# Optimization experiments

Hardware: AMD Instinct MI355X
Metric: run time of the kernel (lower is better)

The kernel has to match this reference:

```python
import jax, jax.numpy as jnp
import numpy as np

B, T, D = 4, 4096, 1024
N, L = 2048, 768
H = 16
EPS = 1e-5

def layernorm(x, g, b):
    mu = jnp.mean(x, axis=-1, keepdims=True)
    var = jnp.mean((x - mu) ** 2, axis=-1, keepdims=True)
    return (x - mu) * jax.lax.rsqrt(var + EPS) * g + b

def setup_inputs() -> dict:
    key = jax.random.key(0)
    ks = jax.random.split(key, 8)
    s_d = 1.0 / np.sqrt(D)
    s_l = 1.0 / np.sqrt(L)
    return {
        "x1": jax.random.normal(ks[0], (B, T, D), jnp.float32),
        "x2": jax.random.normal(ks[1], (B, N, L), jnp.float32),
        "Wq": jax.random.normal(ks[2], (D, D), jnp.float32) * s_d,
        "bq": jnp.zeros((D,), jnp.float32),
        "Wk": jax.random.normal(ks[3], (L, D), jnp.float32) * s_l,
        "bk": jnp.zeros((D,), jnp.float32),
        "Wv": jax.random.normal(ks[4], (L, D), jnp.float32) * s_l,
        "bv": jnp.zeros((D,), jnp.float32),
        "Wh": jax.random.normal(ks[5], (D, D), jnp.float32) * s_d,
        "bh": jnp.zeros((D,), jnp.float32),
        "g1": jnp.ones((D,), jnp.float32),
        "b1": jnp.zeros((D,), jnp.float32),
        "g2": jnp.ones((L,), jnp.float32),
        "b2": jnp.zeros((L,), jnp.float32),
    }

def reference(x1, x2, Wq, bq, Wk, bk, Wv, bv, Wh, bh, g1, b1, g2, b2):
    nx1 = layernorm(x1, g1, b1)
    nx2 = layernorm(x2, g2, b2)
    q = (nx1 @ Wq + bq).reshape(B, T, H, D // H)
    k = (nx2 @ Wk + bk).reshape(B, N, H, D // H)
    v = (nx2 @ Wv + bv).reshape(B, N, H, D // H)
    q = jax.nn.softmax(q, axis=-1)
    k = jax.nn.softmax(k, axis=-1)
    # dropout p=0 -> identity
    attn = jnp.einsum('bnhd,bnhl->bhdl', k, v)          # [B,H,dh,dh]
    y = jnp.einsum('bthd,bhdl->bthl', q, attn).reshape(B, T, D)
    return x1 @ Wh + bh + y
```

## Files before the change

### kernel.cpp

```cpp
#include <hip/hip_runtime.h>


#define DEV __device__ __forceinline__

typedef unsigned short bf16_t;
typedef __attribute__((ext_vector_type(8))) __bf16 bf16x8;
typedef __attribute__((ext_vector_type(8))) unsigned short ushort8;
typedef __attribute__((ext_vector_type(4))) float f32x4;

DEV unsigned short f2bf(float f) {
  unsigned int u = __float_as_uint(f);
  unsigned int r = 0x7FFFu + ((u >> 16) & 1u);
  return (unsigned short)((u + r) >> 16);
}
DEV float bf2f(unsigned short u) { return __uint_as_float(((unsigned int)u) << 16); }

DEV void gld16(const void* g, void* l) {
  __builtin_amdgcn_global_load_lds((__attribute__((address_space(1))) void*)g,
                                   (__attribute__((address_space(3))) void*)l, 16, 0, 0);
}

__global__ __launch_bounds__(256) void prep_kernel(
    const float* __restrict__ Wq, const float* __restrict__ Wk,
    const float* __restrict__ Wv, const float* __restrict__ Wh,
    bf16_t* __restrict__ Wqf, bf16_t* __restrict__ Wkf,
    bf16_t* __restrict__ Wvf, bf16_t* __restrict__ Whf,
    const float* __restrict__ x1, const float* __restrict__ g1,
    const float* __restrict__ b1, bf16_t* __restrict__ nx1f,
    bf16_t* __restrict__ x1f,
    const float* __restrict__ x2, const float* __restrict__ g2,
    const float* __restrict__ b2, bf16_t* __restrict__ nx2f) {
  __shared__ __align__(16) char smem[16 * 1032 * 2];
  __shared__ float murs[16][2];
  int blk = blockIdx.x, tid = threadIdx.x;

  if (blk < 3584) {
    int t = blk;
    const float* src; bf16_t* dst; int KB;
    if (t < 1024)      { src = Wq; dst = Wqf; KB = 32; }
    else if (t < 1792) { src = Wk; dst = Wkf; KB = 24; t -= 1024; }
    else if (t < 2560) { src = Wv; dst = Wvf; KB = 24; t -= 1792; }
    else               { src = Wh; dst = Whf; KB = 32; t -= 2560; }
    int tk = t >> 5, tn = t & 31;
    float (*tile)[33] = (float(*)[33])smem;
    int tx = tid & 31, ty = tid >> 5;
#pragma unroll
    for (int i = 0; i < 4; ++i) {
      int r = ty + i * 8;
      tile[r][tx] = src[(size_t)(tk * 32 + r) * 1024 + tn * 32 + tx];
    }
    __syncthreads();
    if (tid < 128) {
      int rt = tid >> 6, p = (tid >> 4) & 3, ri = tid & 15;
      ushort8 v;
#pragma unroll
      for (int ko = 0; ko < 8; ++ko)
        v[ko] = f2bf(tile[p * 8 + ko][rt * 16 + ri]);
      size_t off = ((size_t)(tn * 2 + rt) * KB + tk) * 512 + p * 128 + ri * 8;
      *(ushort8*)&dst[off] = v;
    }
    return;
  }

  if (blk < 4608) {
    bf16_t* stash = (bf16_t*)smem;
    int rt = blk - 3584;
    {
      int rowl = tid >> 4, ci = tid & 15;
      size_t base = ((size_t)rt * 16 + rowl) * 1024;
      float s = 0.f, s2 = 0.f;
#pragma unroll
      for (int j = 0; j < 16; ++j) {
        int k0 = ci * 4 + j * 64;
        float4 f = *(const float4*)&x1[base + k0];
        s += f.x + f.y + f.z + f.w;
        s2 += f.x * f.x + f.y * f.y + f.z * f.z + f.w * f.w;
        ushort4 u;
        u.x = f2bf(f.x); u.y = f2bf(f.y); u.z = f2bf(f.z); u.w = f2bf(f.w);
        *(ushort4*)&stash[rowl * 1032 + k0] = u;
      }
#pragma unroll
      for (int off = 1; off < 16; off <<= 1) {
        s  += __shfl_xor(s, off);
        s2 += __shfl_xor(s2, off);
      }
      if (ci == 0) {
        float mu = s * (1.0f / 1024.0f);
        float var = s2 * (1.0f / 1024.0f) - mu * mu;
        murs[rowl][0] = mu;
        murs[rowl][1] = rsqrtf(var + 1e-5f);
      }
    }
    __syncthreads();
    {
      int ri = tid & 15, pg = tid >> 4;
      float mu = murs[ri][0], rs = murs[ri][1];
#pragma unroll
      for (int t = 0; t < 8; ++t) {
        int P = pg * 8 + t;
        ushort8 raw = *(const ushort8*)&stash[ri * 1032 + P * 8];
        float4 ga = *(const float4*)&g1[P * 8], gb = *(const float4*)&g1[P * 8 + 4];
        float4 ba = *(const float4*)&b1[P * 8], bb = *(const float4*)&b1[P * 8 + 4];
        float gv[8] = {ga.x, ga.y, ga.z, ga.w, gb.x, gb.y, gb.z, gb.w};
        float bv[8] = {ba.x, ba.y, ba.z, ba.w, bb.x, bb.y, bb.z, bb.w};
        ushort8 nv;
#pragma unroll
        for (int ko = 0; ko < 8; ++ko)
          nv[ko] = f2bf((bf2f(raw[ko]) - mu) * rs * gv[ko] + bv[ko]);
        size_t off = ((size_t)rt * 32 + (P >> 2)) * 512 + (P & 3) * 128 + ri * 8;
        *(ushort8*)&nx1f[off] = nv;
        *(ushort8*)&x1f[off] = raw;
      }
    }
    return;
  }

  {
    bf16_t* stash = (bf16_t*)smem;
    int rt = blk - 4608;
    {
      int rowl = tid >> 4, ci = tid & 15;
      size_t base = ((size_t)rt * 16 + rowl) * 768;
      float s = 0.f, s2 = 0.f;
#pragma unroll
      for (int j = 0; j < 12; ++j) {
        int k0 = ci * 4 + j * 64;
        float4 f = *(const float4*)&x2[base + k0];
        s += f.x + f.y + f.z + f.w;
        s2 += f.x * f.x + f.y * f.y + f.z * f.z + f.w * f.w;
        ushort4 u;
        u.x = f2bf(f.x); u.y = f2bf(f.y); u.z = f2bf(f.z); u.w = f2bf(f.w);
        *(ushort4*)&stash[rowl * 776 + k0] = u;
      }
#pragma unroll
      for (int off = 1; off < 16; off <<= 1) {
        s  += __shfl_xor(s, off);
        s2 += __shfl_xor(s2, off);
      }
      if (ci == 0) {
        float mu = s * (1.0f / 768.0f);
        float var = s2 * (1.0f / 768.0f) - mu * mu;
        murs[rowl][0] = mu;
        murs[rowl][1] = rsqrtf(var + 1e-5f);
      }
    }
    __syncthreads();
    {
      int ri = tid & 15, pg = tid >> 4;
      float mu = murs[ri][0], rs = murs[ri][1];
#pragma unroll
      for (int t = 0; t < 6; ++t) {
        int P = pg * 6 + t;
        ushort8 raw = *(const ushort8*)&stash[ri * 776 + P * 8];
        float4 ga = *(const float4*)&g2[P * 8], gb = *(const float4*)&g2[P * 8 + 4];
        float4 ba = *(const float4*)&b2[P * 8], bb = *(const float4*)&b2[P * 8 + 4];
        float gv[8] = {ga.x, ga.y, ga.z, ga.w, gb.x, gb.y, gb.z, gb.w};
        float bv[8] = {ba.x, ba.y, ba.z, ba.w, bb.x, bb.y, bb.z, bb.w};
        ushort8 nv;
#pragma unroll
        for (int ko = 0; ko < 8; ++ko)
          nv[ko] = f2bf((bf2f(raw[ko]) - mu) * rs * gv[ko] + bv[ko]);
        size_t off = ((size_t)rt * 24 + (P >> 2)) * 512 + (P & 3) * 128 + ri * 8;
        *(ushort8*)&nx2f[off] = nv;
      }
    }
  }
}

__global__ __launch_bounds__(256, 2) void gemm_qkv_kernel(
    const bf16_t* __restrict__ nx1f, const bf16_t* __restrict__ Wqf,
    const float* __restrict__ bq, bf16_t* __restrict__ qout,
    const bf16_t* __restrict__ nx2f, const bf16_t* __restrict__ Wkf,
    const float* __restrict__ bk, bf16_t* __restrict__ kout,
    const bf16_t* __restrict__ Wvf, const float* __restrict__ bv,
    bf16_t* __restrict__ vout) {
  __shared__ bf16_t Bs[2 * 16 * 512];
  int id = blockIdx.x;
  const bf16_t *A, *BT; const float* bias; bf16_t* out;
  int nk, bm, bn, do_softmax;
  if (id < 512) {
    A = nx1f; BT = Wqf; bias = bq; out = qout; nk = 32;
    bm = id & 127; bn = id >> 7; do_softmax = 1;
  } else if (id < 768) {
    id -= 512; A = nx2f; BT = Wkf; bias = bk; out = kout; nk = 24;
    bm = id & 63; bn = id >> 6; do_softmax = 1;
  } else {
    id -= 768; A = nx2f; BT = Wvf; bias = bv; out = vout; nk = 24;
    bm = id & 63; bn = id >> 6; do_softmax = 0;
  }
  int tid = threadIdx.x, lane = tid & 63, wid = tid >> 6;
  int wm = wid & 1, wn = wid >> 1;

  const bf16_t* ap[4];
#pragma unroll
  for (int mi = 0; mi < 4; ++mi)
    ap[mi] = A + ((size_t)(bm * 8 + wm * 4 + mi) * nk) * 512 + lane * 8;
  const bf16_t* sp[4];
#pragma unroll
  for (int i = 0; i < 4; ++i)
    sp[i] = BT + ((size_t)(bn * 16 + wid * 4 + i) * nk) * 512 + lane * 8;

  f32x4 acc[4][8];
#pragma unroll
  for (int i = 0; i < 4; ++i)
#pragma unroll
    for (int j = 0; j < 8; ++j) acc[i][j] = {0.f, 0.f, 0.f, 0.f};

  bf16x8 acur[4], anxt[4];
#pragma unroll
  for (int i = 0; i < 4; ++i)
    gld16(sp[i], (void*)&Bs[(wid * 4 + i) * 512 + lane * 8]);
#pragma unroll
  for (int mi = 0; mi < 4; ++mi) acur[mi] = *(const bf16x8*)ap[mi];

  for (int kt = 0; kt < nk; ++kt) {
    int cb = kt & 1;
    if (kt + 1 < nk) {
      int nb = cb ^ 1;
#pragma unroll
      for (int i = 0; i < 4; ++i)
        gld16(sp[i] + (kt + 1) * 512, (void*)&Bs[nb * 8192 + (wid * 4 + i) * 512 + lane * 8]);
#pragma unroll
      for (int mi = 0; mi < 4; ++mi) anxt[mi] = *(const bf16x8*)(ap[mi] + (kt + 1) * 512);
      asm volatile("s_waitcnt vmcnt(8)\n\ts_barrier" ::: "memory");
    } else {
      asm volatile("s_waitcnt vmcnt(0)\n\ts_barrier" ::: "memory");
    }
    bf16x8 bfr[8];
#pragma unroll
    for (int ni = 0; ni < 8; ++ni)
      bfr[ni] = *(const bf16x8*)&Bs[cb * 8192 + (wn * 8 + ni) * 512 + lane * 8];
#pragma unroll
    for (int mi = 0; mi < 4; ++mi)
#pragma unroll
      for (int ni = 0; ni < 8; ++ni)
        acc[mi][ni] = __builtin_amdgcn_mfma_f32_16x16x32_bf16(acur[mi], bfr[ni], acc[mi][ni], 0, 0, 0);
    asm volatile("s_waitcnt lgkmcnt(0)\n\ts_barrier" ::: "memory");
#pragma unroll
    for (int mi = 0; mi < 4; ++mi) acur[mi] = anxt[mi];
  }

  int colg0 = bn * 256 + wn * 128;
  float bvv[8];
#pragma unroll
  for (int ni = 0; ni < 8; ++ni) bvv[ni] = bias[colg0 + ni * 16 + (lane & 15)];
#pragma unroll
  for (int mi = 0; mi < 4; ++mi) {
#pragma unroll
    for (int r = 0; r < 4; ++r) {
      int row = bm * 128 + wm * 64 + mi * 16 + (lane >> 4) * 4 + r;
      float vx[8];
#pragma unroll
      for (int ni = 0; ni < 8; ++ni) vx[ni] = acc[mi][ni][r] + bvv[ni];
      if (do_softmax) {
#pragma unroll
        for (int g = 0; g < 2; ++g) {
          float ssum = 0.f;
#pragma unroll
          for (int j = 0; j < 4; ++j) { vx[g * 4 + j] = __expf(vx[g * 4 + j]); ssum += vx[g * 4 + j]; }
#pragma unroll
          for (int off = 1; off < 16; off <<= 1) ssum += __shfl_xor(ssum, off);
          float inv = 1.0f / ssum;
#pragma unroll
          for (int j = 0; j < 4; ++j) vx[g * 4 + j] *= inv;
        }
      }
#pragma unroll
      for (int ni = 0; ni < 8; ++ni)
        out[(size_t)row * 1024 + colg0 + ni * 16 + (lane & 15)] = f2bf(vx[ni]);
    }
  }
}

__global__ __launch_bounds__(256) void attn_partial_kernel(
    const bf16_t* __restrict__ kq, const bf16_t* __restrict__ vq,
    float* __restrict__ part) {
  int bh = blockIdx.x >> 3, c = blockIdx.x & 7;
  int b = bh >> 4, h = bh & 15;
  int tid = threadIdx.x, lane = tid & 63, wid = tid >> 6;
  __shared__ bf16_t Kt[64][40];
  __shared__ bf16_t Vt[64][40];
  f32x4 acc[4];
#pragma unroll
  for (int ni = 0; ni < 4; ++ni) acc[ni] = {0.f, 0.f, 0.f, 0.f};
  int nl = tid & 31, d0 = (tid >> 5) * 8;
  int m = lane & 15, kp = lane >> 4;

  for (int s = 0; s < 8; ++s) {
    int n = c * 256 + s * 32 + nl;
    size_t goff = ((size_t)(b * 2048 + n)) * 1024 + h * 64 + d0;
    ushort8 lk = *(const ushort8*)&kq[goff];
    ushort8 lv = *(const ushort8*)&vq[goff];
    __syncthreads();
#pragma unroll
    for (int j = 0; j < 8; ++j) {
      Kt[d0 + j][nl] = lk[j];
      Vt[d0 + j][nl] = lv[j];
    }
    __syncthreads();
    bf16x8 af = *(const bf16x8*)&Kt[wid * 16 + m][kp * 8];
#pragma unroll
    for (int ni = 0; ni < 4; ++ni) {
      bf16x8 bf = *(const bf16x8*)&Vt[ni * 16 + m][kp * 8];
      acc[ni] = __builtin_amdgcn_mfma_f32_16x16x32_bf16(af, bf, acc[ni], 0, 0, 0);
    }
  }
#pragma unroll
  for (int ni = 0; ni < 4; ++ni)
#pragma unroll
    for (int r = 0; r < 4; ++r) {
      int d = wid * 16 + kp * 4 + r;
      int l = ni * 16 + m;
      part[(((size_t)bh * 8 + c) * 64 + d) * 64 + l] = acc[ni][r];
    }
}

__global__ __launch_bounds__(256) void attn_finalize_kernel(
    const float* __restrict__ part, bf16_t* __restrict__ attnT) {
  int bh = blockIdx.x, tid = threadIdx.x;
  for (int t = tid; t < 4096; t += 256) {
    int d = t >> 6, l = t & 63;
    float s = 0.f;
#pragma unroll
    for (int c = 0; c < 8; ++c)
      s += part[(((size_t)bh * 8 + c) * 64 + d) * 64 + l];
    attnT[((size_t)bh * 64 + l) * 64 + d] = f2bf(s);
  }
}

__global__ __launch_bounds__(256, 2) void gemm_final_kernel(
    const bf16_t* __restrict__ x1f, const bf16_t* __restrict__ Whf,
    const float* __restrict__ bias, const bf16_t* __restrict__ qb,
    const bf16_t* __restrict__ attnT, float* __restrict__ out) {
  __shared__ bf16_t Bs[2 * 16 * 512];
  const int nk = 32;
  int tid = threadIdx.x;
  int bm = blockIdx.x, bn = blockIdx.y;
  int lane = tid & 63, wid = tid >> 6;
  int wm = wid & 1, wn = wid >> 1;
  int b = bm >> 5;
  int klane = (lane >> 4) * 8;

  const bf16_t* ap[4];
#pragma unroll
  for (int mi = 0; mi < 4; ++mi)
    ap[mi] = x1f + ((size_t)(bm * 8 + wm * 4 + mi) * nk) * 512 + lane * 8;
  const bf16_t* sp[4];
#pragma unroll
  for (int i = 0; i < 4; ++i)
    sp[i] = Whf + ((size_t)(bn * 16 + wid * 4 + i) * nk) * 512 + lane * 8;

  f32x4 acc[4][8];
#pragma unroll
  for (int i = 0; i < 4; ++i)
#pragma unroll
    for (int j = 0; j < 8; ++j) acc[i][j] = {0.f, 0.f, 0.f, 0.f};

  bf16x8 acur[4], anxt[4];
#pragma unroll
  for (int i = 0; i < 4; ++i)
    gld16(sp[i], (void*)&Bs[(wid * 4 + i) * 512 + lane * 8]);
#pragma unroll
  for (int mi = 0; mi < 4; ++mi) acur[mi] = *(const bf16x8*)ap[mi];

  for (int kt = 0; kt < nk; ++kt) {
    int cb = kt & 1;
    if (kt + 1 < nk) {
      int nb = cb ^ 1;
#pragma unroll
      for (int i = 0; i < 4; ++i)
        gld16(sp[i] + (kt + 1) * 512, (void*)&Bs[nb * 8192 + (wid * 4 + i) * 512 + lane * 8]);
#pragma unroll
      for (int mi = 0; mi < 4; ++mi) anxt[mi] = *(const bf16x8*)(ap[mi] + (kt + 1) * 512);
      asm volatile("s_waitcnt vmcnt(8)\n\ts_barrier" ::: "memory");
    } else {
      asm volatile("s_waitcnt vmcnt(0)\n\ts_barrier" ::: "memory");
    }
    bf16x8 bfr[8];
#pragma unroll
    for (int ni = 0; ni < 8; ++ni)
      bfr[ni] = *(const bf16x8*)&Bs[cb * 8192 + (wn * 8 + ni) * 512 + lane * 8];
#pragma unroll
    for (int mi = 0; mi < 4; ++mi)
#pragma unroll
      for (int ni = 0; ni < 8; ++ni)
        acc[mi][ni] = __builtin_amdgcn_mfma_f32_16x16x32_bf16(acur[mi], bfr[ni], acc[mi][ni], 0, 0, 0);
    asm volatile("s_waitcnt lgkmcnt(0)\n\ts_barrier" ::: "memory");
#pragma unroll
    for (int mi = 0; mi < 4; ++mi) acur[mi] = anxt[mi];
  }

  {
    int h0 = bn * 4 + wn * 2;
#pragma unroll
    for (int k2 = 0; k2 < 2; ++k2) {
      bf16x8 aq[2][4], bt[8];
#pragma unroll
      for (int g = 0; g < 2; ++g)
#pragma unroll
        for (int mi = 0; mi < 4; ++mi)
          aq[g][mi] = *(const bf16x8*)(qb
              + (size_t)(bm * 128 + wm * 64 + mi * 16 + (lane & 15)) * 1024
              + (h0 + g) * 64 + k2 * 32 + klane);
#pragma unroll
      for (int ni = 0; ni < 8; ++ni)
        bt[ni] = *(const bf16x8*)(attnT
            + ((size_t)(b * 16 + h0 + (ni >> 2)) * 64 + (ni & 3) * 16 + (lane & 15)) * 64
            + k2 * 32 + klane);
#pragma unroll
      for (int mi = 0; mi < 4; ++mi)
#pragma unroll
        for (int ni = 0; ni < 8; ++ni)
          acc[mi][ni] = __builtin_amdgcn_mfma_f32_16x16x32_bf16(aq[ni >> 2][mi], bt[ni], acc[mi][ni], 0, 0, 0);
    }
  }

  int colg0 = bn * 256 + wn * 128;
  float bvv[8];
#pragma unroll
  for (int ni = 0; ni < 8; ++ni) bvv[ni] = bias[colg0 + ni * 16 + (lane & 15)];
#pragma unroll
  for (int mi = 0; mi < 4; ++mi)
#pragma unroll
    for (int r = 0; r < 4; ++r) {
      int row = bm * 128 + wm * 64 + mi * 16 + (lane >> 4) * 4 + r;
#pragma unroll
      for (int ni = 0; ni < 8; ++ni)
        out[(size_t)row * 1024 + colg0 + ni * 16 + (lane & 15)] = acc[mi][ni][r] + bvv[ni];
    }
}

extern "C" void kernel_launch(void* const* d_in, const int* in_sizes, int n_in,
                              void* d_out, int out_size, void* d_ws, size_t ws_size,
                              hipStream_t stream) {
  const float* x1 = (const float*)d_in[0];
  const float* x2 = (const float*)d_in[1];
  const float* Wq = (const float*)d_in[2];
  const float* bq = (const float*)d_in[3];
  const float* Wk = (const float*)d_in[4];
  const float* bk = (const float*)d_in[5];
  const float* Wv = (const float*)d_in[6];
  const float* bv = (const float*)d_in[7];
  const float* Wh = (const float*)d_in[8];
  const float* bh = (const float*)d_in[9];
  const float* g1 = (const float*)d_in[10];
  const float* b1 = (const float*)d_in[11];
  const float* g2 = (const float*)d_in[12];
  const float* b2 = (const float*)d_in[13];
  float* out = (float*)d_out;

  char* w = (char*)d_ws;
  bf16_t* nx1f = (bf16_t*)w; w += (size_t)16384 * 1024 * 2;
  bf16_t* x1f  = (bf16_t*)w; w += (size_t)16384 * 1024 * 2;
  bf16_t* nx2f = (bf16_t*)w; w += (size_t)8192 * 768 * 2;
  bf16_t* Wqf  = (bf16_t*)w; w += (size_t)1024 * 1024 * 2;
  bf16_t* Wkf  = (bf16_t*)w; w += (size_t)1024 * 768 * 2;
  bf16_t* Wvf  = (bf16_t*)w; w += (size_t)1024 * 768 * 2;
  bf16_t* Whf  = (bf16_t*)w; w += (size_t)1024 * 1024 * 2;
  bf16_t* qb   = (bf16_t*)w; w += (size_t)16384 * 1024 * 2;
  bf16_t* kbuf = (bf16_t*)w; w += (size_t)8192 * 1024 * 2;
  bf16_t* vbuf = (bf16_t*)w; w += (size_t)8192 * 1024 * 2;
  float*  part = (float*)w;  w += (size_t)64 * 8 * 64 * 64 * 4;
  bf16_t* attnT = (bf16_t*)w; w += (size_t)64 * 64 * 64 * 2;

  prep_kernel<<<dim3(5120), dim3(256), 0, stream>>>(
      Wq, Wk, Wv, Wh, Wqf, Wkf, Wvf, Whf,
      x1, g1, b1, nx1f, x1f, x2, g2, b2, nx2f);
  gemm_qkv_kernel<<<dim3(1024), dim3(256), 0, stream>>>(
      nx1f, Wqf, bq, qb, nx2f, Wkf, bk, kbuf, Wvf, bv, vbuf);
  attn_partial_kernel<<<dim3(512), dim3(256), 0, stream>>>(kbuf, vbuf, part);
  attn_finalize_kernel<<<dim3(64), dim3(256), 0, stream>>>(part, attnT);
  gemm_final_kernel<<<dim3(128, 4), dim3(256), 0, stream>>>(x1f, Whf, bh, qb, attnT, out);
}
```

Before: 299.3 us.

## Fuse attention partial and finalize kernels into one per-head kernel

Replaces the two-pass K^T V computation (512 blocks writing fp32 partials, then a 64-block reduction) with a single kernel of 64 blocks of 512 threads. Each block covers one (batch, head) and splits the sequence across two thread groups. Each group prefetches the next K/V tile into registers before the MFMA step. The two groups' accumulators are combined in shared memory, and the result is written directly as transposed bf16. This removes one launch and the fp32 partial buffer round trip, but cuts the grid to 64 blocks that each run 32 serial iterations, which lowers parallelism on a GPU with many CUs.

Result: slower. 322.9 us (+7.9%).

```diff
diff --git a/kernel.cpp b/kernel.cpp
--- a/kernel.cpp
+++ b/kernel.cpp
@@ -272,59 +272,75 @@
   }
 }
 
-__global__ __launch_bounds__(256) void attn_partial_kernel(
+__global__ __launch_bounds__(512) void attn_kernel(
     const bf16_t* __restrict__ kq, const bf16_t* __restrict__ vq,
-    float* __restrict__ part) {
-  int bh = blockIdx.x >> 3, c = blockIdx.x & 7;
+    bf16_t* __restrict__ attnT) {
+  __shared__ __align__(16) char smem[20480];
+  int bh = blockIdx.x;
   int b = bh >> 4, h = bh & 15;
-  int tid = threadIdx.x, lane = tid & 63, wid = tid >> 6;
-  __shared__ bf16_t Kt[64][40];
-  __shared__ bf16_t Vt[64][40];
+  int tid = threadIdx.x;
+  int g = tid >> 8, tl = tid & 255;
+  int lane = tid & 63, wid = (tid >> 6) & 3;
+  bf16_t* KT = (bf16_t*)(smem + g * 10240);
+  bf16_t* VT = KT + 2560;
+  float* Pt = (float*)smem;
+
+  int nr = tl >> 3, col = (tl & 7) * 8;
+  int m = lane & 15, kp = lane >> 4;
+
   f32x4 acc[4];
 #pragma unroll
   for (int ni = 0; ni < 4; ++ni) acc[ni] = {0.f, 0.f, 0.f, 0.f};
-  int nl = tid & 31, d0 = (tid >> 5) * 8;
-  int m = lane & 15, kp = lane >> 4;
-
-  for (int s = 0; s < 8; ++s) {
-    int n = c * 256 + s * 32 + nl;
-    size_t goff = ((size_t)(b * 2048 + n)) * 1024 + h * 64 + d0;
-    ushort8 lk = *(const ushort8*)&kq[goff];
-    ushort8 lv = *(const ushort8*)&vq[goff];
+
+  size_t gbase = ((size_t)(b * 2048 + g * 1024 + nr)) * 1024 + h * 64 + col;
+  ushort8 ck = *(const ushort8*)&kq[gbase];
+  ushort8 cv = *(const ushort8*)&vq[gbase];
+
+  for (int s = 0; s < 32; ++s) {
+    if (s) __syncthreads();
+#pragma unroll
+    for (int j = 0; j < 8; ++j) {
+      KT[(col + j) * 40 + nr] = (bf16_t)ck[j];
+      VT[(col + j) * 40 + nr] = (bf16_t)cv[j];
+    }
+    if (s + 1 < 32) {
+      size_t go = gbase + (size_t)(s + 1) * 32 * 1024;
+      ck = *(const ushort8*)&kq[go];
+      cv = *(const ushort8*)&vq[go];
+    }
     __syncthreads();
-#pragma unroll
-    for (int j = 0; j < 8; ++j) {
-      Kt[d0 + j][nl] = lk[j];
-      Vt[d0 + j][nl] = lv[j];
-    }
-    __syncthreads();
-    bf16x8 af = *(const bf16x8*)&Kt[wid * 16 + m][kp * 8];
+    bf16x8 af = *(const bf16x8*)&KT[(wid * 16 + m) * 40 + kp * 8];
 #pragma unroll
     for (int ni = 0; ni < 4; ++ni) {
-      bf16x8 bf = *(const bf16x8*)&Vt[ni * 16 + m][kp * 8];
+      bf16x8 bf = *(const bf16x8*)&VT[(ni * 16 + m) * 40 + kp * 8];
       acc[ni] = __builtin_amdgcn_mfma_f32_16x16x32_bf16(af, bf, acc[ni], 0, 0, 0);
     }
   }
-#pragma unroll
-  for (int ni = 0; ni < 4; ++ni)
-#pragma unroll
-    for (int r = 0; r < 4; ++r) {
-      int d = wid * 16 + kp * 4 + r;
-      int l = ni * 16 + m;
-      part[(((size_t)bh * 8 + c) * 64 + d) * 64 + l] = acc[ni][r];
-    }
-}
-
-__global__ __launch_bounds__(256) void attn_finalize_kernel(
-    const float* __restrict__ part, bf16_t* __restrict__ attnT) {
-  int bh = blockIdx.x, tid = threadIdx.x;
-  for (int t = tid; t < 4096; t += 256) {
-    int d = t >> 6, l = t & 63;
-    float s = 0.f;
-#pragma unroll
-    for (int c = 0; c < 8; ++c)
-      s += part[(((size_t)bh * 8 + c) * 64 + d) * 64 + l];
-    attnT[((size_t)bh * 64 + l) * 64 + d] = f2bf(s);
+  __syncthreads();
+  if (g == 0) {
+#pragma unroll
+    for (int ni = 0; ni < 4; ++ni)
+#pragma unroll
+      for (int r = 0; r < 4; ++r)
+        Pt[(ni * 16 + m) * 68 + wid * 16 + kp * 4 + r] = acc[ni][r];
+  }
+  __syncthreads();
+  if (g == 1) {
+#pragma unroll
+    for (int ni = 0; ni < 4; ++ni)
+#pragma unroll
+      for (int r = 0; r < 4; ++r)
+        Pt[(ni * 16 + m) * 68 + wid * 16 + kp * 4 + r] += acc[ni][r];
+  }
+  __syncthreads();
+  {
+    int l = tid >> 3, d0 = (tid & 7) * 8;
+    float4 pa = *(const float4*)&Pt[l * 68 + d0];
+    float4 pb = *(const float4*)&Pt[l * 68 + d0 + 4];
+    ushort8 o;
+    o[0] = f2bf(pa.x); o[1] = f2bf(pa.y); o[2] = f2bf(pa.z); o[3] = f2bf(pa.w);
+    o[4] = f2bf(pb.x); o[5] = f2bf(pb.y); o[6] = f2bf(pb.z); o[7] = f2bf(pb.w);
+    *(ushort8*)&attnT[((size_t)bh * 64 + l) * 64 + d0] = o;
   }
 }
 
@@ -460,7 +476,6 @@
   bf16_t* qb   = (bf16_t*)w; w += (size_t)16384 * 1024 * 2;
   bf16_t* kbuf = (bf16_t*)w; w += (size_t)8192 * 1024 * 2;
   bf16_t* vbuf = (bf16_t*)w; w += (size_t)8192 * 1024 * 2;
-  float*  part = (float*)w;  w += (size_t)64 * 8 * 64 * 64 * 4;
   bf16_t* attnT = (bf16_t*)w; w += (size_t)64 * 64 * 64 * 2;
 
   prep_kernel<<<dim3(5120), dim3(256), 0, stream>>>(
@@ -468,7 +483,6 @@
       x1, g1, b1, nx1f, x1f, x2, g2, b2, nx2f);
   gemm_qkv_kernel<<<dim3(1024), dim3(256), 0, stream>>>(
       nx1f, Wqf, bq, qb, nx2f, Wkf, bk, kbuf, Wvf, bv, vbuf);
-  attn_partial_kernel<<<dim3(512), dim3(256), 0, stream>>>(kbuf, vbuf, part);
-  attn_finalize_kernel<<<dim3(64), dim3(256), 0, stream>>>(part, attnT);
+  attn_kernel<<<dim3(64), dim3(512), 0, stream>>>(kbuf, vbuf, attnT);
   gemm_final_kernel<<<dim3(128, 4), dim3(256), 0, stream>>>(x1f, Whf, bh, qb, attnT, out);
 }
```

## Reconstruct x1 @ Wh from normalized nx1 to drop the x1 bf16 copy

Applied to the files above, without the earlier changes.

Drops the separate bf16 copy of raw x1 and instead feeds the normalized nx1 buffer into the final GEMM. Raw x1 is recovered algebraically via x1 = sd*(nx1 - b1)/g1 + mu: Wh is pre-divided by g1, and per-row mu/sd plus per-column Wh sums are applied in the epilogue. This removes a 32 MB write in the prep kernel and frees workspace. It adds a small column-sum kernel section and per-row stats traffic, but it divides by g1 (which breaks if any g1 is zero) and adds bf16 rounding error from the normalized values.

Measured after the change: 371.3 us. +24.0%, slower.

```diff
diff --git a/kernel.cpp b/kernel.cpp
--- a/kernel.cpp
+++ b/kernel.cpp
@@ -27,27 +27,44 @@
     bf16_t* __restrict__ Wvf, bf16_t* __restrict__ Whf,
     const float* __restrict__ x1, const float* __restrict__ g1,
     const float* __restrict__ b1, bf16_t* __restrict__ nx1f,
-    bf16_t* __restrict__ x1f,
+    float* __restrict__ murs_g,
     const float* __restrict__ x2, const float* __restrict__ g2,
-    const float* __restrict__ b2, bf16_t* __restrict__ nx2f) {
+    const float* __restrict__ b2, bf16_t* __restrict__ nx2f,
+    float* __restrict__ csumd) {
   __shared__ __align__(16) char smem[16 * 1032 * 2];
   __shared__ float murs[16][2];
   int blk = blockIdx.x, tid = threadIdx.x;
 
+  if (blk >= 5120) {
+    int col = (blk - 5120) * 256 + tid;
+    float s0 = 0.f, s1 = 0.f, d0 = 0.f, d1 = 0.f;
+    for (int k = 0; k < 1024; k += 2) {
+      float w0 = Wh[(size_t)k * 1024 + col];
+      float w1 = Wh[(size_t)(k + 1) * 1024 + col];
+      float q0 = b1[k] / g1[k], q1 = b1[k + 1] / g1[k + 1];
+      s0 += w0; s1 += w1; d0 += q0 * w0; d1 += q1 * w1;
+    }
+    csumd[col] = s0 + s1;
+    csumd[1024 + col] = d0 + d1;
+    return;
+  }
+
   if (blk < 3584) {
     int t = blk;
-    const float* src; bf16_t* dst; int KB;
+    const float* src; bf16_t* dst; int KB, is_wh = 0;
     if (t < 1024)      { src = Wq; dst = Wqf; KB = 32; }
     else if (t < 1792) { src = Wk; dst = Wkf; KB = 24; t -= 1024; }
     else if (t < 2560) { src = Wv; dst = Wvf; KB = 24; t -= 1792; }
-    else               { src = Wh; dst = Whf; KB = 32; t -= 2560; }
+    else               { src = Wh; dst = Whf; KB = 32; t -= 2560; is_wh = 1; }
     int tk = t >> 5, tn = t & 31;
     float (*tile)[33] = (float(*)[33])smem;
     int tx = tid & 31, ty = tid >> 5;
 #pragma unroll
     for (int i = 0; i < 4; ++i) {
       int r = ty + i * 8;
-      tile[r][tx] = src[(size_t)(tk * 32 + r) * 1024 + tn * 32 + tx];
+      float v = src[(size_t)(tk * 32 + r) * 1024 + tn * 32 + tx];
+      if (is_wh) v /= g1[tk * 32 + r];
+      tile[r][tx] = v;
     }
     __syncthreads();
     if (tid < 128) {
@@ -87,8 +104,12 @@
       if (ci == 0) {
         float mu = s * (1.0f / 1024.0f);
         float var = s2 * (1.0f / 1024.0f) - mu * mu;
+        float rs = rsqrtf(var + 1e-5f);
         murs[rowl][0] = mu;
-        murs[rowl][1] = rsqrtf(var + 1e-5f);
+        murs[rowl][1] = rs;
+        int row = rt * 16 + rowl;
+        murs_g[row * 2] = mu;
+        murs_g[row * 2 + 1] = 1.0f / rs;
       }
     }
     __syncthreads();
@@ -109,7 +130,6 @@
           nv[ko] = f2bf((bf2f(raw[ko]) - mu) * rs * gv[ko] + bv[ko]);
         size_t off = ((size_t)rt * 32 + (P >> 2)) * 512 + (P & 3) * 128 + ri * 8;
         *(ushort8*)&nx1f[off] = nv;
-        *(ushort8*)&x1f[off] = raw;
       }
     }
     return;
@@ -329,9 +349,10 @@
 }
 
 __global__ __launch_bounds__(256, 2) void gemm_final_kernel(
-    const bf16_t* __restrict__ x1f, const bf16_t* __restrict__ Whf,
+    const bf16_t* __restrict__ nx1f, const bf16_t* __restrict__ Whf,
     const float* __restrict__ bias, const bf16_t* __restrict__ qb,
-    const bf16_t* __restrict__ attnT, float* __restrict__ out) {
+    const bf16_t* __restrict__ attnT, const float* __restrict__ murs_g,
+    const float* __restrict__ csumd, float* __restrict__ out) {
   __shared__ bf16_t Bs[2 * 16 * 512];
   const int nk = 32;
   int tid = threadIdx.x;
@@ -344,7 +365,7 @@
   const bf16_t* ap[4];
 #pragma unroll
   for (int mi = 0; mi < 4; ++mi)
-    ap[mi] = x1f + ((size_t)(bm * 8 + wm * 4 + mi) * nk) * 512 + lane * 8;
+    ap[mi] = nx1f + ((size_t)(bm * 8 + wm * 4 + mi) * nk) * 512 + lane * 8;
   const bf16_t* sp[4];
 #pragma unroll
   for (int i = 0; i < 4; ++i)
@@ -390,6 +411,23 @@
     for (int mi = 0; mi < 4; ++mi) acur[mi] = anxt[mi];
   }
 
+  float mur[4][4], sdr[4][4];
+#pragma unroll
+  for (int mi = 0; mi < 4; ++mi)
+#pragma unroll
+    for (int r = 0; r < 4; ++r) {
+      int row = bm * 128 + wm * 64 + mi * 16 + (lane >> 4) * 4 + r;
+      float2 ms = *(const float2*)&murs_g[row * 2];
+      mur[mi][r] = ms.x; sdr[mi][r] = ms.y;
+    }
+#pragma unroll
+  for (int mi = 0; mi < 4; ++mi)
+#pragma unroll
+    for (int ni = 0; ni < 8; ++ni)
+#pragma unroll
+      for (int r = 0; r < 4; ++r)
+        acc[mi][ni][r] *= sdr[mi][r];
+
   {
     int h0 = bn * 4 + wn * 2;
 #pragma unroll
@@ -416,9 +454,14 @@
   }
 
   int colg0 = bn * 256 + wn * 128;
-  float bvv[8];
-#pragma unroll
-  for (int ni = 0; ni < 8; ++ni) bvv[ni] = bias[colg0 + ni * 16 + (lane & 15)];
+  float bvv[8], csv[8], dvv[8];
+#pragma unroll
+  for (int ni = 0; ni < 8; ++ni) {
+    int col = colg0 + ni * 16 + (lane & 15);
+    bvv[ni] = bias[col];
+    csv[ni] = csumd[col];
+    dvv[ni] = csumd[1024 + col];
+  }
 #pragma unroll
   for (int mi = 0; mi < 4; ++mi)
 #pragma unroll
@@ -426,7 +469,8 @@
       int row = bm * 128 + wm * 64 + mi * 16 + (lane >> 4) * 4 + r;
 #pragma unroll
       for (int ni = 0; ni < 8; ++ni)
-        out[(size_t)row * 1024 + colg0 + ni * 16 + (lane & 15)] = acc[mi][ni][r] + bvv[ni];
+        out[(size_t)row * 1024 + colg0 + ni * 16 + (lane & 15)] =
+            acc[mi][ni][r] + mur[mi][r] * csv[ni] - sdr[mi][r] * dvv[ni] + bvv[ni];
     }
 }
 
@@ -451,7 +495,6 @@
 
   char* w = (char*)d_ws;
   bf16_t* nx1f = (bf16_t*)w; w += (size_t)16384 * 1024 * 2;
-  bf16_t* x1f  = (bf16_t*)w; w += (size_t)16384 * 1024 * 2;
   bf16_t* nx2f = (bf16_t*)w; w += (size_t)8192 * 768 * 2;
   bf16_t* Wqf  = (bf16_t*)w; w += (size_t)1024 * 1024 * 2;
   bf16_t* Wkf  = (bf16_t*)w; w += (size_t)1024 * 768 * 2;
@@ -462,13 +505,16 @@
   bf16_t* vbuf = (bf16_t*)w; w += (size_t)8192 * 1024 * 2;
   float*  part = (float*)w;  w += (size_t)64 * 8 * 64 * 64 * 4;
   bf16_t* attnT = (bf16_t*)w; w += (size_t)64 * 64 * 64 * 2;
-
-  prep_kernel<<<dim3(5120), dim3(256), 0, stream>>>(
+  float*  murs  = (float*)w; w += (size_t)16384 * 2 * 4;
+  float*  csumd = (float*)w; w += (size_t)2048 * 4;
+
+  prep_kernel<<<dim3(5124), dim3(256), 0, stream>>>(
       Wq, Wk, Wv, Wh, Wqf, Wkf, Wvf, Whf,
-      x1, g1, b1, nx1f, x1f, x2, g2, b2, nx2f);
+      x1, g1, b1, nx1f, murs, x2, g2, b2, nx2f, csumd);
   gemm_qkv_kernel<<<dim3(1024), dim3(256), 0, stream>>>(
       nx1f, Wqf, bq, qb, nx2f, Wkf, bk, kbuf, Wvf, bv, vbuf);
   attn_partial_kernel<<<dim3(512), dim3(256), 0, stream>>>(kbuf, vbuf, part);
   attn_finalize_kernel<<<dim3(64), dim3(256), 0, stream>>>(part, attnT);
-  gemm_final_kernel<<<dim3(128, 4), dim3(256), 0, stream>>>(x1f, Whf, bh, qb, attnT, out);
-}
+  gemm_final_kernel<<<dim3(128, 4), dim3(256), 0, stream>>>(
+      nx1f, Whf, bh, qb, attnT, murs, csumd, out);
+}
```
